# Kernel optimization log

Measured on AMD Instinct MI355X. Metric: run time of the kernel, lower is better.

The kernel has to match this reference:

```python
import jax, jax.numpy as jnp
import numpy as np
import math

H, DK, G_DIM, S_DIM, HID = 8, 64, 512, 3072, 512
B = 16384
EPS = 1e-5

def _layernorm(x, g, b):
    mu = jnp.mean(x, axis=-1, keepdims=True)
    var = jnp.mean((x - mu) ** 2, axis=-1, keepdims=True)
    return (x - mu) * jax.lax.rsqrt(var + EPS) * g + b

def setup_inputs() -> dict:
    key = jax.random.key(0)
    ks = jax.random.split(key, 12)
    s = 0.02
    return {
        "h_g": jax.random.normal(ks[0], (B, G_DIM), jnp.float32),
        "h_s": jax.random.normal(ks[1], (B, S_DIM), jnp.float32),
        # stacked per-head projections: [H, in_dim, d_k]
        "Wq": jax.random.normal(ks[2], (H, G_DIM, DK), jnp.float32) * s,
        "bq": jnp.zeros((H, DK), jnp.float32),
        "Wk": jax.random.normal(ks[3], (H, S_DIM, DK), jnp.float32) * s,
        "bk": jnp.zeros((H, DK), jnp.float32),
        "Wv": jax.random.normal(ks[4], (H, S_DIM, DK), jnp.float32) * s,
        "bv": jnp.zeros((H, DK), jnp.float32),
        "Wo": jax.random.normal(ks[5], (HID, HID), jnp.float32) * s,
        "bo": jnp.zeros((HID,), jnp.float32),
        "ln1_g": jnp.ones((HID,), jnp.float32),
        "ln1_b": jnp.zeros((HID,), jnp.float32),
        "W1": jax.random.normal(ks[6], (HID, 2 * HID), jnp.float32) * s,
        "b1": jnp.zeros((2 * HID,), jnp.float32),
        "W2": jax.random.normal(ks[7], (2 * HID, HID), jnp.float32) * s,
        "b2": jnp.zeros((HID,), jnp.float32),
        "ln2_g": jnp.ones((HID,), jnp.float32),
        "ln2_b": jnp.zeros((HID,), jnp.float32),
    }

def reference(h_g, h_s, Wq, bq, Wk, bk, Wv, bv, Wo, bo, ln1_g, ln1_b, W1, b1, W2, b2, ln2_g, ln2_b):
    b = h_g.shape[0]
    # batched per-head projections (fuses the per-head Linear loop)
    Q = jnp.einsum('bg,hgd->bhd', h_g, Wq) + bq          # [B,H,DK]
    K = jnp.einsum('bs,hsd->bhd', h_s, Wk) + bk          # [B,H,DK]
    V = jnp.einsum('bs,hsd->bhd', h_s, Wv) + bv          # [B,H,DK]
    # seq_len == 1: scores is [B,H,1]; softmax over a single key == 1
    scores = jnp.sum(Q * K, axis=-1, keepdims=True) / math.sqrt(DK)
    attn_w = jax.nn.softmax(scores, axis=-1)             # identically ones
    attn = attn_w * V                                    # == V
    h_concat = attn.reshape(b, H * DK)                   # [B,HID]
    h_attn = h_concat @ Wo + bo
    h_attn = _layernorm(h_attn + h_g, ln1_g, ln1_b)
    # MLP (dropout is identity in eval mode); torch GELU default = exact erf
    h = jax.nn.gelu(h_attn @ W1 + b1, approximate=False) @ W2 + b2
    return _layernorm(h + h_attn, ln2_g, ln2_b)
```

## Files before the change

### kernel.cpp

```cpp
#include <hip/hip_runtime.h>
#include <hip/hip_bf16.h>
#include <math.h>

#define HH    8
#define DKK   64
#define GD    512
#define SD    3072
#define HID_  512
#define BB    16384

typedef unsigned short ushort_t;
typedef __attribute__((ext_vector_type(8))) short bf16x8;
typedef __attribute__((ext_vector_type(4))) float f32x4;

__device__ __forceinline__ float bf2f(ushort_t u) {
  union { unsigned int i; float f; } c; c.i = ((unsigned int)u) << 16; return c.f;
}
__device__ __forceinline__ ushort_t f2bf(float f) {
  union { float f; unsigned int i; } c; c.f = f;
  unsigned int x = c.i;
  return (ushort_t)((x + 0x7FFFu + ((x >> 16) & 1u)) >> 16);
}
__device__ __forceinline__ unsigned int pk_bf16(float a, float b) {
  __hip_bfloat162 h = __float22bfloat162_rn(make_float2(a, b));
  union { __hip_bfloat162 h; unsigned int u; } c; c.h = h; return c.u;
}

__device__ __forceinline__ void async_cp16(const ushort_t* gsrc, ushort_t* ldst) {
  __builtin_amdgcn_global_load_lds(
      (const __attribute__((address_space(1))) unsigned int*)gsrc,
      (__attribute__((address_space(3))) unsigned int*)ldst, 16, 0, 0);
}
__device__ __forceinline__ void async_cp16f(const float* gsrc, float* ldst) {
  __builtin_amdgcn_global_load_lds(
      (const __attribute__((address_space(1))) unsigned int*)gsrc,
      (__attribute__((address_space(3))) unsigned int*)ldst, 16, 0, 0);
}

__device__ __forceinline__ float gelu_tanh(float x) {
  float y = 0.79788456080286535588f * (x + 0.044715f * x * x * x);
  float e = __expf(2.0f * y);
  float th = 1.0f - 2.0f / (e + 1.0f);
  return 0.5f * x * (1.0f + th);
}

__device__ __forceinline__ void swz_coords(int& nb, int& mb, int& kz) {
  int NB = gridDim.x, MB = gridDim.y;
  int bid = blockIdx.x + NB * (blockIdx.y + MB * blockIdx.z);
  int xcd = bid & 7;
  int j = bid >> 3;
  nb = j & (NB - 1);
  int rest = j / NB;
  int mk = (rest << 3) | xcd;
  mb = mk & (MB - 1);
  kz = mk / MB;
}

template <int EPI, int SWZ>
__global__ __launch_bounds__(256) void gemm_bt(
    const ushort_t* __restrict__ A, const ushort_t* __restrict__ Bt,
    void* __restrict__ Cv, const float* __restrict__ bias,
    int M, int N, int Kfull, int Klen) {
  __shared__ __align__(16) ushort_t As[2][128 * 32];
  __shared__ __align__(16) ushort_t Bs[2][128 * 32];
  const int tid = threadIdx.x;
  const int wv = tid >> 6;
  const int lane = tid & 63;
  int nb, mb, kz;
  if (SWZ) swz_coords(nb, mb, kz);
  else { nb = blockIdx.x; mb = blockIdx.y; kz = blockIdx.z; }
  const int m0 = mb * 128, n0 = nb * 128, kbeg = kz * Klen;
  const int srow = lane >> 2;
  const int scol = (lane & 3) * 8;
  const int wm = wv & 1, wn = wv >> 1;
  const int lr = lane & 15, quad = lane >> 4;

  f32x4 acc[4][4];
#pragma unroll
  for (int i = 0; i < 4; ++i)
#pragma unroll
    for (int j = 0; j < 4; ++j) acc[i][j] = (f32x4){0.f, 0.f, 0.f, 0.f};

  const ushort_t* Ab = A + (size_t)m0 * Kfull + kbeg;
  const ushort_t* Bb = Bt + (size_t)n0 * Kfull + kbeg;

  auto stage = [&](int k0, int b) {
#pragma unroll
    for (int i = 0; i < 2; ++i) {
      const int chunk = i * 4 + wv;
      const int row = chunk * 16 + srow;
      async_cp16(Ab + (size_t)row * Kfull + (k0 + scol), &As[b][chunk * 512]);
      async_cp16(Bb + (size_t)row * Kfull + (k0 + scol), &Bs[b][chunk * 512]);
    }
  };

  const int nt = Klen >> 5;
  stage(0, 0);
  int buf = 0;
  for (int t = 0; t < nt; ++t, buf ^= 1) {
    __syncthreads();
    if (t + 1 < nt) stage((t + 1) << 5, buf ^ 1);
    bf16x8 af[4], bfr[4];
#pragma unroll
    for (int i = 0; i < 4; ++i)
      af[i] = *(const bf16x8*)&As[buf][(wm * 64 + i * 16 + lr) * 32 + quad * 8];
#pragma unroll
    for (int j = 0; j < 4; ++j)
      bfr[j] = *(const bf16x8*)&Bs[buf][(wn * 64 + j * 16 + lr) * 32 + quad * 8];
#pragma unroll
    for (int i = 0; i < 4; ++i)
#pragma unroll
      for (int j = 0; j < 4; ++j)
        acc[i][j] = __builtin_amdgcn_mfma_f32_16x16x32_bf16(af[i], bfr[j], acc[i][j], 0, 0, 0);
  }

#pragma unroll
  for (int i = 0; i < 4; ++i) {
    const int mg = m0 + wm * 64 + i * 16 + quad * 4;
#pragma unroll
    for (int j = 0; j < 4; ++j) {
      const int ng = n0 + wn * 64 + j * 16 + lr;
      if (EPI == 2) {
        float* C = (float*)Cv + (size_t)kz * M * N;
#pragma unroll
        for (int r = 0; r < 4; ++r)
          C[(size_t)(mg + r) * N + ng] = acc[i][j][r];
      } else {
        ushort_t* C = (ushort_t*)Cv;
        const float bvv = bias ? bias[ng] : 0.0f;
#pragma unroll
        for (int r = 0; r < 4; ++r) {
          float v = acc[i][j][r] + bvv;
          if (EPI == 1) v = gelu_tanh(v);
          C[(size_t)(mg + r) * N + ng] = f2bf(v);
        }
      }
    }
  }
}

__global__ __launch_bounds__(256, 4) void gemm_a32(
    const float* __restrict__ A, const ushort_t* __restrict__ Bt,
    float* __restrict__ C, int M, int N, int Kfull, int Klen) {
  __shared__ __align__(16) float As4[2][128 * 32];
  __shared__ __align__(16) ushort_t Bs[2][128 * 32];
  const int tid = threadIdx.x;
  const int wv = tid >> 6;
  const int lane = tid & 63;
  int nb, mb, kz;
  swz_coords(nb, mb, kz);
  const int m0 = mb * 128, n0 = nb * 128, kbeg = kz * Klen;
  const int srow = lane >> 2;
  const int scol = (lane & 3) * 8;
  const int wm = wv & 1, wn = wv >> 1;
  const int lr = lane & 15, quad = lane >> 4;
  const int a_rc = lane >> 3;
  const int a_g = (lane & 7) ^ a_rc;

  f32x4 acc[4][4];
#pragma unroll
  for (int i = 0; i < 4; ++i)
#pragma unroll
    for (int j = 0; j < 4; ++j) acc[i][j] = (f32x4){0.f, 0.f, 0.f, 0.f};

  const float* Ab = A + (size_t)m0 * Kfull + kbeg;
  const ushort_t* Bb = Bt + (size_t)n0 * Kfull + kbeg;

  auto stage = [&](int k0, int b) {
#pragma unroll
    for (int i = 0; i < 2; ++i) {
      const int chunk = i * 4 + wv;
      const int row = chunk * 16 + srow;
      async_cp16(Bb + (size_t)row * Kfull + (k0 + scol), &Bs[b][chunk * 512]);
    }
#pragma unroll
    for (int t4 = 0; t4 < 4; ++t4) {
      const int chunkA = t4 * 4 + wv;
      const int r = chunkA * 8 + a_rc;
      async_cp16f(Ab + (size_t)r * Kfull + (k0 + 4 * a_g), &As4[b][chunkA * 256]);
    }
  };

  const int nt = Klen >> 5;
  stage(0, 0);
  int buf = 0;
  for (int t = 0; t < nt; ++t, buf ^= 1) {
    __syncthreads();
    if (t + 1 < nt) stage((t + 1) << 5, buf ^ 1);
    bf16x8 af[4], bfr[4];
#pragma unroll
    for (int i = 0; i < 4; ++i) {
      const int r = wm * 64 + i * 16 + lr;
      const int x0 = (2 * quad) ^ (lr & 7);
      const int x1 = (2 * quad + 1) ^ (lr & 7);
      float4 fa = *(const float4*)&As4[buf][r * 32 + x0 * 4];
      float4 fb = *(const float4*)&As4[buf][r * 32 + x1 * 4];
      union { unsigned int u[4]; bf16x8 v; } c;
      c.u[0] = pk_bf16(fa.x, fa.y); c.u[1] = pk_bf16(fa.z, fa.w);
      c.u[2] = pk_bf16(fb.x, fb.y); c.u[3] = pk_bf16(fb.z, fb.w);
      af[i] = c.v;
    }
#pragma unroll
    for (int j = 0; j < 4; ++j)
      bfr[j] = *(const bf16x8*)&Bs[buf][(wn * 64 + j * 16 + lr) * 32 + quad * 8];
#pragma unroll
    for (int i = 0; i < 4; ++i)
#pragma unroll
      for (int j = 0; j < 4; ++j)
        acc[i][j] = __builtin_amdgcn_mfma_f32_16x16x32_bf16(af[i], bfr[j], acc[i][j], 0, 0, 0);
  }

  float* Cp = C + (size_t)kz * M * N;
#pragma unroll
  for (int i = 0; i < 4; ++i) {
    const int mg = m0 + wm * 64 + i * 16 + quad * 4;
#pragma unroll
    for (int j = 0; j < 4; ++j) {
      const int ng = n0 + wn * 64 + j * 16 + lr;
#pragma unroll
      for (int r = 0; r < 4; ++r)
        Cp[(size_t)(mg + r) * N + ng] = acc[i][j][r];
    }
  }
}

__global__ __launch_bounds__(256) void permute_wv(const float* __restrict__ Wv,
                                                  ushort_t* __restrict__ Wvp) {
  const int idx = (blockIdx.x * 256 + threadIdx.x) * 8;
  const int s = idx >> 9;
  const int c = idx & 511;
  const float* src = Wv + (size_t)(c >> 6) * (SD * DKK) + (size_t)s * DKK + (c & 63);
  float4 a = *(const float4*)src;
  float4 b = *(const float4*)(src + 4);
  unsigned int p[4];
  p[0] = pk_bf16(a.x, a.y); p[1] = pk_bf16(a.z, a.w);
  p[2] = pk_bf16(b.x, b.y); p[3] = pk_bf16(b.z, b.w);
  *(uint4*)(Wvp + idx) = *(const uint4*)p;
}

__global__ __launch_bounds__(256) void transpose3(
    const float* __restrict__ s0, ushort_t* __restrict__ d0,
    const float* __restrict__ s1, ushort_t* __restrict__ d1,
    const float* __restrict__ s2, ushort_t* __restrict__ d2) {
  __shared__ ushort_t tile[32][33];
  const int z = blockIdx.z;
  const float* src = (z == 0) ? s0 : (z == 1) ? s1 : s2;
  ushort_t* dst = (z == 0) ? d0 : (z == 1) ? d1 : d2;
  const int R = (z == 2) ? 1024 : 512;
  const int C = (z == 1) ? 1024 : 512;
  const int bx = blockIdx.x * 32;
  const int by = blockIdx.y * 32;
  if (bx >= C || by >= R) return;
  const int tx = threadIdx.x, ty = threadIdx.y;
#pragma unroll
  for (int i = 0; i < 32; i += 8)
    tile[ty + i][tx] = f2bf(src[(size_t)(by + ty + i) * C + (bx + tx)]);
  __syncthreads();
#pragma unroll
  for (int i = 0; i < 32; i += 8)
    dst[(size_t)(bx + ty + i) * R + (by + tx)] = tile[tx][ty + i];
}

__global__ __launch_bounds__(256) void c0_kernel(const float* __restrict__ bv,
                                                 const float* __restrict__ Wo,
                                                 const float* __restrict__ bo,
                                                 float* __restrict__ c0) {
  __shared__ float red[8][32];
  const int jl = threadIdx.x & 31;
  const int chunk = threadIdx.x >> 5;
  const int j = blockIdx.x * 32 + jl;
  const int cbase = chunk * 64;
  float s = 0.f;
#pragma unroll 8
  for (int c = 0; c < 64; ++c) s += bv[cbase + c] * Wo[(size_t)(cbase + c) * 512 + j];
  red[chunk][jl] = s;
  __syncthreads();
  if (chunk == 0) {
    float t = bo[j];
#pragma unroll
    for (int q = 0; q < 8; ++q) t += red[q][jl];
    c0[j] = t;
  }
}

template <int RES_F32, int OUT_F32>
__global__ __launch_bounds__(256) void ln_fused(const float* __restrict__ p0,
                                                const float* __restrict__ p1,
                                                const float* __restrict__ cb,
                                                const void* __restrict__ res_,
                                                const float* __restrict__ g,
                                                const float* __restrict__ b,
                                                void* __restrict__ out_) {
  const int row = blockIdx.x * 4 + (threadIdx.x >> 6);
  const int lane = threadIdx.x & 63;
  const size_t base = (size_t)row * 512 + lane * 8;
  const int col = lane * 8;
  float4 a0 = *(const float4*)(p0 + base);
  float4 a1 = *(const float4*)(p0 + base + 4);
  float4 c0v = *(const float4*)(p1 + base);
  float4 c1v = *(const float4*)(p1 + base + 4);
  float4 d0 = *(const float4*)(cb + col);
  float4 d1 = *(const float4*)(cb + col + 4);
  float t[8];
  t[0] = a0.x + c0v.x + d0.x; t[1] = a0.y + c0v.y + d0.y;
  t[2] = a0.z + c0v.z + d0.z; t[3] = a0.w + c0v.w + d0.w;
  t[4] = a1.x + c1v.x + d1.x; t[5] = a1.y + c1v.y + d1.y;
  t[6] = a1.z + c1v.z + d1.z; t[7] = a1.w + c1v.w + d1.w;
  float r[8];
  if (RES_F32) {
    const float* res = (const float*)res_;
    float4 e0 = *(const float4*)(res + base);
    float4 e1 = *(const float4*)(res + base + 4);
    r[0] = e0.x; r[1] = e0.y; r[2] = e0.z; r[3] = e0.w;
    r[4] = e1.x; r[5] = e1.y; r[6] = e1.z; r[7] = e1.w;
  } else {
    const ushort_t* res = (const ushort_t*)res_;
    uint4 rv = *(const uint4*)(res + base);
    const ushort_t* rp = (const ushort_t*)&rv;
#pragma unroll
    for (int k = 0; k < 8; ++k) r[k] = bf2f(rp[k]);
  }
  float x[8];
  float s = 0.f, sq = 0.f;
#pragma unroll
  for (int k = 0; k < 8; ++k) {
    float v = t[k] + r[k];
    x[k] = v; s += v; sq += v * v;
  }
#pragma unroll
  for (int off = 32; off > 0; off >>= 1) {
    s += __shfl_xor(s, off);
    sq += __shfl_xor(sq, off);
  }
  const float mean = s * (1.0f / 512.0f);
  const float var = sq * (1.0f / 512.0f) - mean * mean;
  const float rstd = rsqrtf(var + 1e-5f);
  float4 gv0 = *(const float4*)(g + col);
  float4 gv1 = *(const float4*)(g + col + 4);
  float4 bv0 = *(const float4*)(b + col);
  float4 bv1 = *(const float4*)(b + col + 4);
  const float gg[8] = {gv0.x, gv0.y, gv0.z, gv0.w, gv1.x, gv1.y, gv1.z, gv1.w};
  const float bb[8] = {bv0.x, bv0.y, bv0.z, bv0.w, bv1.x, bv1.y, bv1.z, bv1.w};
  float y[8];
#pragma unroll
  for (int k = 0; k < 8; ++k) y[k] = (x[k] - mean) * rstd * gg[k] + bb[k];
  if (OUT_F32) {
    float* out = (float*)out_;
    *(float4*)(out + base) = make_float4(y[0], y[1], y[2], y[3]);
    *(float4*)(out + base + 4) = make_float4(y[4], y[5], y[6], y[7]);
  } else {
    ushort_t* out = (ushort_t*)out_;
    uint4 ov; ushort_t* op = (ushort_t*)&ov;
#pragma unroll
    for (int k = 0; k < 8; ++k) op[k] = f2bf(y[k]);
    *(uint4*)(out + base) = ov;
  }
}

extern "C" void kernel_launch(void* const* d_in, const int* in_sizes, int n_in,
                              void* d_out, int out_size, void* d_ws, size_t ws_size,
                              hipStream_t stream) {
  const float* h_g  = (const float*)d_in[0];
  const float* h_s  = (const float*)d_in[1];
  const float* Wv   = (const float*)d_in[6];
  const float* bv   = (const float*)d_in[7];
  const float* Wo   = (const float*)d_in[8];
  const float* bo   = (const float*)d_in[9];
  const float* ln1g = (const float*)d_in[10];
  const float* ln1b = (const float*)d_in[11];
  const float* W1   = (const float*)d_in[12];
  const float* b1   = (const float*)d_in[13];
  const float* W2   = (const float*)d_in[14];
  const float* b2   = (const float*)d_in[15];
  const float* ln2g = (const float*)d_in[16];
  const float* ln2b = (const float*)d_in[17];

  char* ws = (char*)d_ws;
  ushort_t* WoT = (ushort_t*)(ws + 0);
  ushort_t* W1T = (ushort_t*)(ws + 524288);
  ushort_t* W2T = (ushort_t*)(ws + 1572864);
  ushort_t* Wvp = (ushort_t*)(ws + 2621440);
  ushort_t* WcT = (ushort_t*)(ws + 5767168);
  float*    c0f = (float*)(ws + 8912896);
  float*    p0  = (float*)(ws + 16777216);
  float*    p1  = (float*)(ws + 50331648);
  ushort_t* x   = (ushort_t*)(ws + 83886080);
  ushort_t* u   = (ushort_t*)(ws + 100663296);
  float*    q0  = p0;
  float*    q1  = p1;
  (void)in_sizes; (void)n_in; (void)out_size; (void)ws_size;

  hipLaunchKernelGGL(permute_wv, dim3(768), dim3(256), 0, stream, Wv, Wvp);
  hipLaunchKernelGGL(transpose3, dim3(32, 32, 3), dim3(32, 8), 0, stream,
                     Wo, WoT, W1, W1T, W2, W2T);
  hipLaunchKernelGGL(c0_kernel, dim3(16), dim3(256), 0, stream, bv, Wo, bo, c0f);

  hipLaunchKernelGGL((gemm_bt<0, 0>), dim3(24, 4, 1), dim3(256), 0, stream,
                     WoT, Wvp, (void*)WcT, (const float*)nullptr, 512, 3072, 512, 512);
  hipLaunchKernelGGL(gemm_a32, dim3(4, 128, 2), dim3(256), 0, stream,
                     h_s, WcT, p0, BB, 512, 3072, 1536);
  hipLaunchKernelGGL((ln_fused<1, 0>), dim3(4096), dim3(256), 0, stream,
                     p0, p1, c0f, (const void*)h_g, ln1g, ln1b, (void*)x);
  hipLaunchKernelGGL((gemm_bt<1, 1>), dim3(8, 128, 1), dim3(256), 0, stream,
                     x, W1T, (void*)u, b1, BB, 1024, 512, 512);
  hipLaunchKernelGGL((gemm_bt<2, 1>), dim3(4, 128, 2), dim3(256), 0, stream,
                     u, W2T, (void*)q0, (const float*)nullptr, BB, 512, 1024, 512);
  hipLaunchKernelGGL((ln_fused<0, 1>), dim3(4096), dim3(256), 0, stream,
                     q0, q1, b2, (const void*)x, ln2g, ln2b, d_out);
}
```

Baseline: 549.4 us.

## Convert A tile to bf16 once at staging via register prefetch instead of per-wave

The fp32 A operand of gemm_a32 was copied straight into LDS with async loads, and each wave converted it to bf16 on every read. Now each thread loads its A slice into registers for the next k-step, converts it to bf16 once, and writes it to LDS after the MFMA block. This halves LDS footprint and read traffic for A and removes the duplicated conversions. The cost is more live registers and a synchronous global load in the loop, which could lower occupancy under launch_bounds(256,4).

Measured after the change: 583.0 us. 6.1% more time.

```diff
diff --git a/kernel.cpp b/kernel.cpp
--- a/kernel.cpp
+++ b/kernel.cpp
@@ -27,11 +27,6 @@
 }
 
 __device__ __forceinline__ void async_cp16(const ushort_t* gsrc, ushort_t* ldst) {
-  __builtin_amdgcn_global_load_lds(
-      (const __attribute__((address_space(1))) unsigned int*)gsrc,
-      (__attribute__((address_space(3))) unsigned int*)ldst, 16, 0, 0);
-}
-__device__ __forceinline__ void async_cp16f(const float* gsrc, float* ldst) {
   __builtin_amdgcn_global_load_lds(
       (const __attribute__((address_space(1))) unsigned int*)gsrc,
       (__attribute__((address_space(3))) unsigned int*)ldst, 16, 0, 0);
@@ -142,7 +137,7 @@
 __global__ __launch_bounds__(256, 4) void gemm_a32(
     const float* __restrict__ A, const ushort_t* __restrict__ Bt,
     float* __restrict__ C, int M, int N, int Kfull, int Klen) {
-  __shared__ __align__(16) float As4[2][128 * 32];
+  __shared__ __align__(16) ushort_t As[2][128 * 32];
   __shared__ __align__(16) ushort_t Bs[2][128 * 32];
   const int tid = threadIdx.x;
   const int wv = tid >> 6;
@@ -154,8 +149,11 @@
   const int scol = (lane & 3) * 8;
   const int wm = wv & 1, wn = wv >> 1;
   const int lr = lane & 15, quad = lane >> 4;
-  const int a_rc = lane >> 3;
-  const int a_g = (lane & 7) ^ a_rc;
+  const int a_r0 = tid >> 2;
+  const int a_gl = tid & 3;
+  const int a_ph = a_gl ^ (a_r0 & 3);
+  const int a_w0 = a_r0 * 32 + a_ph * 8;
+  const int a_w1 = (a_r0 + 64) * 32 + a_ph * 8;
 
   f32x4 acc[4][4];
 #pragma unroll
@@ -166,40 +164,51 @@
   const float* Ab = A + (size_t)m0 * Kfull + kbeg;
   const ushort_t* Bb = Bt + (size_t)n0 * Kfull + kbeg;
 
-  auto stage = [&](int k0, int b) {
+  float4 pre0, pre1, pre2, pre3;
+  auto loadA = [&](int k0) {
+    const float* pa = Ab + (size_t)a_r0 * Kfull + (k0 + a_gl * 8);
+    const float* pb = Ab + (size_t)(a_r0 + 64) * Kfull + (k0 + a_gl * 8);
+    pre0 = *(const float4*)pa;
+    pre1 = *(const float4*)(pa + 4);
+    pre2 = *(const float4*)pb;
+    pre3 = *(const float4*)(pb + 4);
+  };
+  auto writeA = [&](int b) {
+    unsigned int u0[4], u1[4];
+    u0[0] = pk_bf16(pre0.x, pre0.y); u0[1] = pk_bf16(pre0.z, pre0.w);
+    u0[2] = pk_bf16(pre1.x, pre1.y); u0[3] = pk_bf16(pre1.z, pre1.w);
+    u1[0] = pk_bf16(pre2.x, pre2.y); u1[1] = pk_bf16(pre2.z, pre2.w);
+    u1[2] = pk_bf16(pre3.x, pre3.y); u1[3] = pk_bf16(pre3.z, pre3.w);
+    *(uint4*)&As[b][a_w0] = *(const uint4*)u0;
+    *(uint4*)&As[b][a_w1] = *(const uint4*)u1;
+  };
+  auto stageB = [&](int k0, int b) {
 #pragma unroll
     for (int i = 0; i < 2; ++i) {
       const int chunk = i * 4 + wv;
       const int row = chunk * 16 + srow;
       async_cp16(Bb + (size_t)row * Kfull + (k0 + scol), &Bs[b][chunk * 512]);
     }
-#pragma unroll
-    for (int t4 = 0; t4 < 4; ++t4) {
-      const int chunkA = t4 * 4 + wv;
-      const int r = chunkA * 8 + a_rc;
-      async_cp16f(Ab + (size_t)r * Kfull + (k0 + 4 * a_g), &As4[b][chunkA * 256]);
-    }
   };
 
+  loadA(0);
+  stageB(0, 0);
+  writeA(0);
+
+  const int acol = (quad ^ (lr & 3)) * 8;
   const int nt = Klen >> 5;
-  stage(0, 0);
   int buf = 0;
   for (int t = 0; t < nt; ++t, buf ^= 1) {
     __syncthreads();
-    if (t + 1 < nt) stage((t + 1) << 5, buf ^ 1);
+    const bool pf = (t + 1 < nt);
+    if (pf) {
+      stageB((t + 1) << 5, buf ^ 1);
+      loadA((t + 1) << 5);
+    }
     bf16x8 af[4], bfr[4];
 #pragma unroll
-    for (int i = 0; i < 4; ++i) {
-      const int r = wm * 64 + i * 16 + lr;
-      const int x0 = (2 * quad) ^ (lr & 7);
-      const int x1 = (2 * quad + 1) ^ (lr & 7);
-      float4 fa = *(const float4*)&As4[buf][r * 32 + x0 * 4];
-      float4 fb = *(const float4*)&As4[buf][r * 32 + x1 * 4];
-      union { unsigned int u[4]; bf16x8 v; } c;
-      c.u[0] = pk_bf16(fa.x, fa.y); c.u[1] = pk_bf16(fa.z, fa.w);
-      c.u[2] = pk_bf16(fb.x, fb.y); c.u[3] = pk_bf16(fb.z, fb.w);
-      af[i] = c.v;
-    }
+    for (int i = 0; i < 4; ++i)
+      af[i] = *(const bf16x8*)&As[buf][(wm * 64 + i * 16 + lr) * 32 + acol];
 #pragma unroll
     for (int j = 0; j < 4; ++j)
       bfr[j] = *(const bf16x8*)&Bs[buf][(wn * 64 + j * 16 + lr) * 32 + quad * 8];
@@ -208,6 +217,7 @@
 #pragma unroll
       for (int j = 0; j < 4; ++j)
         acc[i][j] = __builtin_amdgcn_mfma_f32_16x16x32_bf16(af[i], bfr[j], acc[i][j], 0, 0, 0);
+    if (pf) writeA(buf ^ 1);
   }
 
   float* Cp = C + (size_t)kz * M * N;
```
